# Performance work log

Hardware: AMD Instinct MI355X
Metric: run time of the kernel (lower is better)

## Reference

```python
import jax, jax.numpy as jnp
import numpy as np

B, S, HID = 2, 2048, 2048
H, KVH, D = 16, 4, 128
GROUPS = H // KVH  # 4


def apply_rotary(x, cos, sin):
    # x: [B, h, S, D]; cos/sin: [S, D//2]
    xr = x[..., 0::2]
    xi = x[..., 1::2]
    c = cos[None, None, :, :]
    s = sin[None, None, :, :]
    orr = xr * c - xi * s
    oi = xr * s + xi * c
    return jnp.stack([orr, oi], axis=-1).reshape(x.shape)


def setup_inputs() -> dict:
    key = jax.random.key(0)
    k0, k1, k2, k3, k4 = jax.random.split(key, 5)
    x = jax.random.normal(k0, (B, S, HID), dtype=jnp.float32)
    # real RoPE frequencies (llama-style), stored as [S, D//2, 2] = (cos, sin)
    inv_freq = 1.0 / (10000.0 ** (np.arange(0, D, 2, dtype=np.float32) / D))
    t = np.arange(S, dtype=np.float32)
    ang = np.outer(t, inv_freq)  # [S, D//2]
    freqs_cis = jnp.asarray(np.stack([np.cos(ang), np.sin(ang)], axis=-1), dtype=jnp.float32)
    sc = 0.02
    wq = jax.random.normal(k1, (HID, H * D), dtype=jnp.float32) * sc
    wk = jax.random.normal(k2, (HID, KVH * D), dtype=jnp.float32) * sc
    wv = jax.random.normal(k3, (HID, KVH * D), dtype=jnp.float32) * sc
    wo = jax.random.normal(k4, (H * D, HID), dtype=jnp.float32) * sc
    return {"x": x, "freqs_cis": freqs_cis, "wq": wq, "wk": wk, "wv": wv, "wo": wo}


def reference(x, freqs_cis, wq, wk, wv, wo):
    b, s, _ = x.shape
    cos, sin = freqs_cis[..., 0], freqs_cis[..., 1]
    q = (x @ wq).reshape(b, s, H, D).transpose(0, 2, 1, 3)    # [B,H,S,D]
    k = (x @ wk).reshape(b, s, KVH, D).transpose(0, 2, 1, 3)  # [B,KVH,S,D]
    v = (x @ wv).reshape(b, s, KVH, D).transpose(0, 2, 1, 3)
    q = apply_rotary(q, cos, sin)
    k = apply_rotary(k, cos, sin)
    # GQA expand: repeat kv heads into query-head groups
    k = jnp.repeat(k, GROUPS, axis=1)  # [B,H,S,D]
    v = jnp.repeat(v, GROUPS, axis=1)
    scale = 1.0 / jnp.sqrt(jnp.asarray(D, dtype=x.dtype))
    scores = jnp.einsum("bhqd,bhkd->bhqk", q, k) * scale
    causal = jnp.tril(jnp.ones((s, s), dtype=bool))
    scores = jnp.where(causal[None, None], scores, jnp.asarray(-jnp.inf, dtype=scores.dtype))
    attn = jax.nn.softmax(scores, axis=-1)
    out = jnp.einsum("bhqk,bhkd->bhqd", attn, v)
    out = out.transpose(0, 2, 1, 3).reshape(b, s, H * D)
    return out @ wo
```

## Files before the change

kernel.cpp:

```cpp
#include <hip/hip_runtime.h>
#include <hip/hip_bf16.h>

#define B_   2
#define S_   2048
#define HID_ 2048
#define H_   16
#define KVH_ 4
#define D_   128
#define M_   4096
#define NQKV 3072

typedef __attribute__((ext_vector_type(8))) short bf16x8;
typedef __attribute__((ext_vector_type(4))) float f32x4;
typedef const __attribute__((address_space(1))) unsigned int* gas_p;
typedef __attribute__((address_space(3))) unsigned int* las_p;

__device__ __forceinline__ unsigned short f2b(float f) {
    __hip_bfloat16 h = __float2bfloat16(f);
    return *reinterpret_cast<unsigned short*>(&h);
}
__device__ __forceinline__ float b2f(unsigned short u) {
    __hip_bfloat16 h;
    *reinterpret_cast<unsigned short*>(&h) = u;
    return __bfloat162float(h);
}

__global__ __launch_bounds__(256)
void convert_x(const float* __restrict__ x, unsigned short* __restrict__ xb) {
    int i = (blockIdx.x * 256 + threadIdx.x) * 4;
    float4 v = *(const float4*)(x + i);
    ushort4 o;
    o.x = f2b(v.x); o.y = f2b(v.y); o.z = f2b(v.z); o.w = f2b(v.w);
    *(ushort4*)(xb + i) = o;
}

__global__ __launch_bounds__(256)
void convert_w_t(const float* __restrict__ w, int N,
                 unsigned short* __restrict__ wt, int nbase) {
    __shared__ float tile[32][33];
    int tx = threadIdx.x & 31, ty = threadIdx.x >> 5;
    int n0 = blockIdx.x * 32, k0 = blockIdx.y * 32;
    #pragma unroll
    for (int j = 0; j < 4; j++)
        tile[ty + j*8][tx] = w[(size_t)(k0 + ty + j*8) * N + n0 + tx];
    __syncthreads();
    #pragma unroll
    for (int j = 0; j < 4; j++)
        wt[(size_t)(nbase + n0 + ty + j*8) * 2048 + k0 + tx] = f2b(tile[tx][ty + j*8]);
}

template<bool BF16OUT>
__global__ __launch_bounds__(256)
void gemm_bt(const unsigned short* __restrict__ A,
             const unsigned short* __restrict__ BT,
             void* __restrict__ Cv, int N) {
    __shared__ unsigned short As[128][32];
    __shared__ unsigned short Bs[128][32];

    int tid  = threadIdx.x;
    int lane = tid & 63, w = tid >> 6;
    int quad = lane >> 4, l15 = lane & 15;
    int row0 = blockIdx.y * 128, col0 = blockIdx.x * 128;
    int wm = (w & 1) * 64, wn = (w >> 1) * 64;

    f32x4 acc[4][4];
    const f32x4 zf = {0.f, 0.f, 0.f, 0.f};
    #pragma unroll
    for (int i = 0; i < 4; i++)
        #pragma unroll
        for (int j = 0; j < 4; j++) acc[i][j] = zf;

    const unsigned short* Arow = A  + (size_t)row0 * 2048;
    const unsigned short* Brow = BT + (size_t)col0 * 2048;

    for (int k0 = 0; k0 < 2048; k0 += 32) {
        #pragma unroll
        for (int it = 0; it < 2; it++) {
            int c = w * 128 + it * 64 + lane;
            int r = c >> 2, q8 = (c & 3) * 8;
            __builtin_amdgcn_global_load_lds(
                (gas_p)(Arow + (size_t)r * 2048 + k0 + q8),
                (las_p)((char*)&As[0][0] + (size_t)(w * 128 + it * 64) * 16),
                16, 0, 0);
            __builtin_amdgcn_global_load_lds(
                (gas_p)(Brow + (size_t)r * 2048 + k0 + q8),
                (las_p)((char*)&Bs[0][0] + (size_t)(w * 128 + it * 64) * 16),
                16, 0, 0);
        }
        __syncthreads();
        bf16x8 af[4], bf[4];
        #pragma unroll
        for (int i = 0; i < 4; i++) af[i] = *(const bf16x8*)&As[wm + i*16 + l15][quad * 8];
        #pragma unroll
        for (int j = 0; j < 4; j++) bf[j] = *(const bf16x8*)&Bs[wn + j*16 + l15][quad * 8];
        #pragma unroll
        for (int i = 0; i < 4; i++)
            #pragma unroll
            for (int j = 0; j < 4; j++)
                acc[i][j] = __builtin_amdgcn_mfma_f32_16x16x32_bf16(af[i], bf[j], acc[i][j], 0, 0, 0);
        __syncthreads();
    }

    #pragma unroll
    for (int i = 0; i < 4; i++)
        #pragma unroll
        for (int j = 0; j < 4; j++)
            #pragma unroll
            for (int r = 0; r < 4; r++) {
                size_t idx = (size_t)(row0 + wm + i*16 + quad*4 + r) * N + col0 + wn + j*16 + l15;
                if (BF16OUT) ((unsigned short*)Cv)[idx] = f2b(acc[i][j][r]);
                else         ((float*)Cv)[idx] = acc[i][j][r];
            }
}

__global__ __launch_bounds__(256)
void rope_kernel(unsigned short* __restrict__ qkv, const float* __restrict__ freqs) {
    int p = blockIdx.x * 256 + threadIdx.x;
    int m = p / 1280;
    int cp = p - m * 1280;
    int col = cp * 2;
    int s = m & (S_ - 1);
    int d = col & (D_ - 1);
    unsigned short* ptr = qkv + (size_t)m * NQKV + col;
    ushort2 uv = *(ushort2*)ptr;
    float xr = b2f(uv.x), xi = b2f(uv.y);
    float cs = freqs[s * 128 + d], sn = freqs[s * 128 + d + 1];
    ushort2 ov;
    ov.x = f2b(xr * cs - xi * sn);
    ov.y = f2b(xr * sn + xi * cs);
    *(ushort2*)ptr = ov;
}

__global__ __launch_bounds__(256)
void v_transpose(const unsigned short* __restrict__ qkv, unsigned short* __restrict__ vT) {
    __shared__ unsigned short tile[32][34];
    int tx = threadIdx.x & 31, ty = threadIdx.x >> 5;
    int s0 = blockIdx.x * 32;
    int c0 = blockIdx.y * 32;
    int b  = blockIdx.z;
    #pragma unroll
    for (int j = 0; j < 4; j++)
        tile[ty + j*8][tx] = qkv[(size_t)(b*2048 + s0 + ty + j*8) * NQKV + 2560 + c0 + tx];
    __syncthreads();
    #pragma unroll
    for (int j = 0; j < 4; j++)
        vT[(size_t)(b*512 + c0 + ty + j*8) * 2048 + s0 + tx] = tile[tx][ty + j*8];
}

__global__ __launch_bounds__(128)
void attn_mfma(const unsigned short* __restrict__ qkv,
               const unsigned short* __restrict__ vT,
               unsigned short* __restrict__ ao,
               unsigned short* __restrict__ wsP,
               float2* __restrict__ wsML) {
    __shared__ unsigned short Ks[64 * 128];
    __shared__ unsigned short Vt[128 * 64];

    int tid  = threadIdx.x;
    int lane = tid & 63, w = tid >> 6;
    int quad = lane >> 4, l15 = lane & 15;
    int bx = blockIdx.x, h = blockIdx.y, b = blockIdx.z;
    int hk = h >> 2;

    int qt, c;
    bool split = (bx < 32);
    if (split) { qt = 31 - (bx >> 1); c = bx & 1; }
    else       { qt = 47 - bx;        c = 0;      }
    int nt = qt + 1;
    int kt_begin = 0, kt_end = nt;
    if (split) {
        int nt0 = (nt + 1) >> 1;
        kt_begin = c ? nt0 : 0;
        kt_end   = c ? nt  : nt0;
    }
    int q0 = qt * 64;
    const float scale = 0.08838834764831845f;

    bf16x8 aq[2][4];
    #pragma unroll
    for (int qf = 0; qf < 2; qf++) {
        const unsigned short* qrow =
            qkv + (size_t)(b*2048 + q0 + w*32 + qf*16 + l15) * NQKV + h*128;
        #pragma unroll
        for (int k4 = 0; k4 < 4; k4++)
            aq[qf][k4] = *(const bf16x8*)(qrow + k4*32 + quad*8);
    }

    int koff[4][4];
    #pragma unroll
    for (int j = 0; j < 4; j++) {
        int row = ((j >> 1) * 32) + ((l15 >> 2) * 8) + ((j & 1) * 4) + (l15 & 3);
        #pragma unroll
        for (int k4 = 0; k4 < 4; k4++) {
            int slot = (k4 * 4 + quad) ^ (row & 15);
            koff[j][k4] = (row * 16 + slot) * 8;
        }
    }
    int vbase0 = (l15 * 8 + (quad ^ (l15 & 7))) * 8;
    int vbase1 = (l15 * 8 + ((4 + quad) ^ (l15 & 7))) * 8;

    const unsigned short* kb0 = qkv + (size_t)(b*2048) * NQKV + 2048 + hk*128;
    const unsigned short* vb0 = vT + (size_t)(b*512 + hk*128) * 2048;

    auto stage_k = [&](int kt) {
        #pragma unroll
        for (int it = 0; it < 8; it++) {
            int s = w * 512 + it * 64 + lane;
            int r = s >> 4, qp = s & 15;
            int q = qp ^ (r & 15);
            __builtin_amdgcn_global_load_lds(
                (gas_p)(kb0 + (size_t)(kt*64 + r) * NQKV + q * 8),
                (las_p)((char*)&Ks[0] + (w * 512 + it * 64) * 16),
                16, 0, 0);
        }
    };
    auto stage_v = [&](int kt) {
        #pragma unroll
        for (int it = 0; it < 8; it++) {
            int s = w * 512 + it * 64 + lane;
            int r = s >> 3, qp = s & 7;
            int q = qp ^ (r & 7);
            __builtin_amdgcn_global_load_lds(
                (gas_p)(vb0 + (size_t)r * 2048 + kt*64 + q * 8),
                (las_p)((char*)&Vt[0] + (w * 512 + it * 64) * 16),
                16, 0, 0);
        }
    };

    f32x4 o_acc[2][8];
    const f32x4 zf = {0.f, 0.f, 0.f, 0.f};
    #pragma unroll
    for (int qf = 0; qf < 2; qf++)
        #pragma unroll
        for (int jn = 0; jn < 8; jn++) o_acc[qf][jn] = zf;
    float m_i[2] = {-1e30f, -1e30f}, l_i[2] = {0.f, 0.f};
    int qglob[2] = {q0 + w*32 + l15, q0 + w*32 + 16 + l15};

    stage_k(kt_begin);
    for (int kt = kt_begin; kt < kt_end; kt++) {
        __syncthreads();
        stage_v(kt);

        f32x4 s_acc[2][4];
        #pragma unroll
        for (int j = 0; j < 4; j++) {
            s_acc[0][j] = zf; s_acc[1][j] = zf;
            #pragma unroll
            for (int k4 = 0; k4 < 4; k4++) {
                bf16x8 ak = *(const bf16x8*)&Ks[koff[j][k4]];
                s_acc[0][j] = __builtin_amdgcn_mfma_f32_16x16x32_bf16(ak, aq[0][k4], s_acc[0][j], 0, 0, 0);
                s_acc[1][j] = __builtin_amdgcn_mfma_f32_16x16x32_bf16(ak, aq[1][k4], s_acc[1][j], 0, 0, 0);
            }
        }

        bf16x8 pp[2][2];
        #pragma unroll
        for (int qf = 0; qf < 2; qf++) {
            float sv[4][4];
            #pragma unroll
            for (int j = 0; j < 4; j++)
                #pragma unroll
                for (int r = 0; r < 4; r++)
                    sv[j][r] = s_acc[qf][j][r] * scale;
            if (kt == qt) {
                #pragma unroll
                for (int j = 0; j < 4; j++)
                    #pragma unroll
                    for (int r = 0; r < 4; r++) {
                        int sloc = ((j >> 1) * 32) + quad*8 + ((j & 1) * 4) + r;
                        if (kt*64 + sloc > qglob[qf]) sv[j][r] = -1e30f;
                    }
            }
            float mx = sv[0][0];
            #pragma unroll
            for (int j = 0; j < 4; j++)
                #pragma unroll
                for (int r = 0; r < 4; r++) mx = fmaxf(mx, sv[j][r]);
            mx = fmaxf(mx, __shfl_xor(mx, 16));
            mx = fmaxf(mx, __shfl_xor(mx, 32));
            float mnew = fmaxf(m_i[qf], mx);
            float alpha = __expf(m_i[qf] - mnew);
            float rs = 0.f;
            float p[4][4];
            #pragma unroll
            for (int j = 0; j < 4; j++)
                #pragma unroll
                for (int r = 0; r < 4; r++) {
                    p[j][r] = __expf(sv[j][r] - mnew);
                    rs += p[j][r];
                }
            l_i[qf] = l_i[qf] * alpha + rs;
            m_i[qf] = mnew;
            #pragma unroll
            for (int jn = 0; jn < 8; jn++)
                #pragma unroll
                for (int r = 0; r < 4; r++) o_acc[qf][jn][r] *= alpha;
            #pragma unroll
            for (int r = 0; r < 4; r++) {
                pp[qf][0][r]     = (short)f2b(p[0][r]);
                pp[qf][0][r + 4] = (short)f2b(p[1][r]);
                pp[qf][1][r]     = (short)f2b(p[2][r]);
                pp[qf][1][r + 4] = (short)f2b(p[3][r]);
            }
        }

        __syncthreads();
        if (kt + 1 < kt_end) stage_k(kt + 1);

        #pragma unroll
        for (int jn = 0; jn < 8; jn++) {
            bf16x8 av0 = *(const bf16x8*)&Vt[jn*1024 + vbase0];
            bf16x8 av1 = *(const bf16x8*)&Vt[jn*1024 + vbase1];
            o_acc[0][jn] = __builtin_amdgcn_mfma_f32_16x16x32_bf16(av0, pp[0][0], o_acc[0][jn], 0, 0, 0);
            o_acc[0][jn] = __builtin_amdgcn_mfma_f32_16x16x32_bf16(av1, pp[0][1], o_acc[0][jn], 0, 0, 0);
            o_acc[1][jn] = __builtin_amdgcn_mfma_f32_16x16x32_bf16(av0, pp[1][0], o_acc[1][jn], 0, 0, 0);
            o_acc[1][jn] = __builtin_amdgcn_mfma_f32_16x16x32_bf16(av1, pp[1][1], o_acc[1][jn], 0, 0, 0);
        }
    }

    int pidx = ((qt - 16) * 16 + h) * 2 + b;
    #pragma unroll
    for (int qf = 0; qf < 2; qf++) {
        float lt = l_i[qf];
        lt += __shfl_xor(lt, 16);
        lt += __shfl_xor(lt, 32);
        float inv = 1.f / lt;
        int q_local = w*32 + qf*16 + l15;
        unsigned short* dst;
        if (!split || c == 1)
            dst = ao + (size_t)(b*2048 + q0 + q_local) * 2048 + h*128;
        else
            dst = wsP + (size_t)pidx * 8192 + q_local * 128;
        #pragma unroll
        for (int jn = 0; jn < 8; jn++) {
            ushort4 ov;
            ov.x = f2b(o_acc[qf][jn][0] * inv);
            ov.y = f2b(o_acc[qf][jn][1] * inv);
            ov.z = f2b(o_acc[qf][jn][2] * inv);
            ov.w = f2b(o_acc[qf][jn][3] * inv);
            *(ushort4*)(dst + jn*16 + quad*4) = ov;
        }
        if (split && quad == 0)
            wsML[(pidx*2 + c) * 64 + q_local] = make_float2(m_i[qf], lt);
    }
}

__global__ __launch_bounds__(256)
void merge_kernel(unsigned short* __restrict__ ao,
                  const unsigned short* __restrict__ wsP,
                  const float2* __restrict__ wsML) {
    int t = blockIdx.x * 256 + threadIdx.x;
    int d  = (t & 15) * 8;
    int h  = (t >> 4) & 15;
    int qg = 1024 + ((t >> 8) & 1023);
    int b  = t >> 18;
    int qt = qg >> 6, q_local = qg & 63;
    int pidx = ((qt - 16) * 16 + h) * 2 + b;

    float2 ml0 = wsML[(pidx*2 + 0) * 64 + q_local];
    float2 ml1 = wsML[(pidx*2 + 1) * 64 + q_local];
    float mm = fmaxf(ml0.x, ml1.x);
    float f0 = __expf(ml0.x - mm) * ml0.y;
    float f1 = __expf(ml1.x - mm) * ml1.y;
    float inv = 1.f / (f0 + f1);
    f0 *= inv; f1 *= inv;

    unsigned short* arow = ao + (size_t)(b*2048 + qg) * 2048 + h*128 + d;
    const unsigned short* prow = wsP + (size_t)pidx * 8192 + q_local * 128 + d;
    ushort4 a0 = *(ushort4*)arow,        a1 = *(ushort4*)(arow + 4);
    ushort4 p0 = *(const ushort4*)prow,  p1 = *(const ushort4*)(prow + 4);
    ushort4 o0, o1;
    o0.x = f2b(f1*b2f(a0.x) + f0*b2f(p0.x));
    o0.y = f2b(f1*b2f(a0.y) + f0*b2f(p0.y));
    o0.z = f2b(f1*b2f(a0.z) + f0*b2f(p0.z));
    o0.w = f2b(f1*b2f(a0.w) + f0*b2f(p0.w));
    o1.x = f2b(f1*b2f(a1.x) + f0*b2f(p1.x));
    o1.y = f2b(f1*b2f(a1.y) + f0*b2f(p1.y));
    o1.z = f2b(f1*b2f(a1.z) + f0*b2f(p1.z));
    o1.w = f2b(f1*b2f(a1.w) + f0*b2f(p1.w));
    *(ushort4*)arow = o0;
    *(ushort4*)(arow + 4) = o1;
}

extern "C" void kernel_launch(void* const* d_in, const int* in_sizes, int n_in,
                              void* d_out, int out_size, void* d_ws, size_t ws_size,
                              hipStream_t stream) {
    const float* x     = (const float*)d_in[0];
    const float* freqs = (const float*)d_in[1];
    const float* wq    = (const float*)d_in[2];
    const float* wk    = (const float*)d_in[3];
    const float* wv    = (const float*)d_in[4];
    const float* wo    = (const float*)d_in[5];
    float* out = (float*)d_out;

    char* ws = (char*)d_ws;
    unsigned short* xbf    = (unsigned short*)(ws);
    unsigned short* aobuf  = (unsigned short*)(ws);
    unsigned short* wqkvT  = (unsigned short*)(ws + (16u<<20));
    unsigned short* woT    = (unsigned short*)(ws + (28u<<20));
    unsigned short* qkvbuf = (unsigned short*)(ws + (36u<<20));
    unsigned short* vTbuf  = (unsigned short*)(ws + (60u<<20));
    unsigned short* wsP    = (unsigned short*)(ws + (16u<<20));
    float2*         wsML   = (float2*)(ws + (24u<<20));

    dim3 blk(256);
    convert_x<<<8192, blk, 0, stream>>>(x, xbf);
    convert_w_t<<<dim3(64, 64), blk, 0, stream>>>(wq, 2048, wqkvT, 0);
    convert_w_t<<<dim3(16, 64), blk, 0, stream>>>(wk,  512, wqkvT, 2048);
    convert_w_t<<<dim3(16, 64), blk, 0, stream>>>(wv,  512, wqkvT, 2560);
    convert_w_t<<<dim3(64, 64), blk, 0, stream>>>(wo, 2048, woT, 0);

    gemm_bt<true><<<dim3(NQKV/128, M_/128), blk, 0, stream>>>(xbf, wqkvT, qkvbuf, NQKV);
    rope_kernel<<<20480, blk, 0, stream>>>(qkvbuf, freqs);
    v_transpose<<<dim3(64, 16, 2), blk, 0, stream>>>(qkvbuf, vTbuf);
    attn_mfma<<<dim3(48, 16, 2), dim3(128), 0, stream>>>(qkvbuf, vTbuf, aobuf, wsP, wsML);
    merge_kernel<<<2048, blk, 0, stream>>>(aobuf, wsP, wsML);
    gemm_bt<false><<<dim3(2048/128, M_/128), blk, 0, stream>>>(aobuf, woT, out, 2048);
}
```

Before: 353.8 us.

## Fuse RoPE and V-transpose into QKV GEMM, share KV tiles across GQA heads

The four weight-conversion launches become one batched launch. RoPE and the V transpose move into the QKV GEMM epilogue, which removes two kernels and their round trips through global memory. The attention kernel now runs 512 threads per block covering all four query heads of a KV head, so each K/V tile staged in LDS is shared across the group. The split-KV scheme is reworked to use up to three chunks of 14 key tiles, and the merge kernel is generalised to match. The trade-offs are more uncoalesced scalar stores and freq loads in the GEMM epilogue and fewer, larger attention blocks.

After: 345.1 us. -2.5%, faster.

```diff
diff --git a/kernel.cpp b/kernel.cpp
--- a/kernel.cpp
+++ b/kernel.cpp
@@ -35,25 +35,35 @@
 }
 
 __global__ __launch_bounds__(256)
-void convert_w_t(const float* __restrict__ w, int N,
-                 unsigned short* __restrict__ wt, int nbase) {
+void convert_w_all(const float* __restrict__ wq, const float* __restrict__ wk,
+                   const float* __restrict__ wv, const float* __restrict__ wo,
+                   unsigned short* __restrict__ wqkvT,
+                   unsigned short* __restrict__ woT) {
     __shared__ float tile[32][33];
+    int z = blockIdx.z;
+    const float* w; int N, nbase; unsigned short* dst;
+    if (z == 0)      { w = wq; N = 2048; nbase = 0;    dst = wqkvT; }
+    else if (z == 1) { w = wk; N = 512;  nbase = 2048; dst = wqkvT; }
+    else if (z == 2) { w = wv; N = 512;  nbase = 2560; dst = wqkvT; }
+    else             { w = wo; N = 2048; nbase = 0;    dst = woT; }
+    int n0 = blockIdx.x * 32, k0 = blockIdx.y * 32;
+    if (n0 >= N) return;
     int tx = threadIdx.x & 31, ty = threadIdx.x >> 5;
-    int n0 = blockIdx.x * 32, k0 = blockIdx.y * 32;
     #pragma unroll
     for (int j = 0; j < 4; j++)
         tile[ty + j*8][tx] = w[(size_t)(k0 + ty + j*8) * N + n0 + tx];
     __syncthreads();
     #pragma unroll
     for (int j = 0; j < 4; j++)
-        wt[(size_t)(nbase + n0 + ty + j*8) * 2048 + k0 + tx] = f2b(tile[tx][ty + j*8]);
-}
-
-template<bool BF16OUT>
+        dst[(size_t)(nbase + n0 + ty + j*8) * 2048 + k0 + tx] = f2b(tile[tx][ty + j*8]);
+}
+
 __global__ __launch_bounds__(256)
-void gemm_bt(const unsigned short* __restrict__ A,
-             const unsigned short* __restrict__ BT,
-             void* __restrict__ Cv, int N) {
+void gemm_qkv(const unsigned short* __restrict__ A,
+              const unsigned short* __restrict__ BT,
+              unsigned short* __restrict__ qkv,
+              unsigned short* __restrict__ vT,
+              const float* __restrict__ freqs) {
     __shared__ unsigned short As[128][32];
     __shared__ unsigned short Bs[128][32];
 
@@ -101,53 +111,106 @@
         __syncthreads();
     }
 
+    bool isV = (col0 >= 2560);
+    #pragma unroll
+    for (int i = 0; i < 4; i++) {
+        int m0 = row0 + wm + i*16 + quad*4;
+        int s0 = m0 & 2047;
+        if (!isV) {
+            #pragma unroll
+            for (int j = 0; j < 4; j++) {
+                int col = col0 + wn + j*16 + l15;
+                int dd = (col & 127) & ~1;
+                bool odd = col & 1;
+                #pragma unroll
+                for (int r = 0; r < 4; r++) {
+                    int s = s0 + r;
+                    float cs = freqs[s*128 + dd];
+                    float sn = freqs[s*128 + dd + 1];
+                    float v  = acc[i][j][r];
+                    float pv = __shfl_xor(v, 1);
+                    float o  = odd ? (pv*sn + v*cs) : (v*cs - pv*sn);
+                    qkv[(size_t)(m0 + r) * NQKV + col] = f2b(o);
+                }
+            }
+        } else {
+            #pragma unroll
+            for (int j = 0; j < 4; j++) {
+                int col = col0 + wn + j*16 + l15;
+                int vrow = (m0 >> 11) * 512 + (col - 2560);
+                ushort4 ov;
+                ov.x = f2b(acc[i][j][0]);
+                ov.y = f2b(acc[i][j][1]);
+                ov.z = f2b(acc[i][j][2]);
+                ov.w = f2b(acc[i][j][3]);
+                *(ushort4*)(vT + (size_t)vrow * 2048 + s0) = ov;
+            }
+        }
+    }
+}
+
+__global__ __launch_bounds__(256)
+void gemm_out(const unsigned short* __restrict__ A,
+              const unsigned short* __restrict__ BT,
+              float* __restrict__ C, int N) {
+    __shared__ unsigned short As[128][32];
+    __shared__ unsigned short Bs[128][32];
+
+    int tid  = threadIdx.x;
+    int lane = tid & 63, w = tid >> 6;
+    int quad = lane >> 4, l15 = lane & 15;
+    int row0 = blockIdx.y * 128, col0 = blockIdx.x * 128;
+    int wm = (w & 1) * 64, wn = (w >> 1) * 64;
+
+    f32x4 acc[4][4];
+    const f32x4 zf = {0.f, 0.f, 0.f, 0.f};
     #pragma unroll
     for (int i = 0; i < 4; i++)
         #pragma unroll
+        for (int j = 0; j < 4; j++) acc[i][j] = zf;
+
+    const unsigned short* Arow = A  + (size_t)row0 * 2048;
+    const unsigned short* Brow = BT + (size_t)col0 * 2048;
+
+    for (int k0 = 0; k0 < 2048; k0 += 32) {
+        #pragma unroll
+        for (int it = 0; it < 2; it++) {
+            int c = w * 128 + it * 64 + lane;
+            int r = c >> 2, q8 = (c & 3) * 8;
+            __builtin_amdgcn_global_load_lds(
+                (gas_p)(Arow + (size_t)r * 2048 + k0 + q8),
+                (las_p)((char*)&As[0][0] + (size_t)(w * 128 + it * 64) * 16),
+                16, 0, 0);
+            __builtin_amdgcn_global_load_lds(
+                (gas_p)(Brow + (size_t)r * 2048 + k0 + q8),
+                (las_p)((char*)&Bs[0][0] + (size_t)(w * 128 + it * 64) * 16),
+                16, 0, 0);
+        }
+        __syncthreads();
+        bf16x8 af[4], bf[4];
+        #pragma unroll
+        for (int i = 0; i < 4; i++) af[i] = *(const bf16x8*)&As[wm + i*16 + l15][quad * 8];
+        #pragma unroll
+        for (int j = 0; j < 4; j++) bf[j] = *(const bf16x8*)&Bs[wn + j*16 + l15][quad * 8];
+        #pragma unroll
+        for (int i = 0; i < 4; i++)
+            #pragma unroll
+            for (int j = 0; j < 4; j++)
+                acc[i][j] = __builtin_amdgcn_mfma_f32_16x16x32_bf16(af[i], bf[j], acc[i][j], 0, 0, 0);
+        __syncthreads();
+    }
+
+    #pragma unroll
+    for (int i = 0; i < 4; i++)
+        #pragma unroll
         for (int j = 0; j < 4; j++)
             #pragma unroll
-            for (int r = 0; r < 4; r++) {
-                size_t idx = (size_t)(row0 + wm + i*16 + quad*4 + r) * N + col0 + wn + j*16 + l15;
-                if (BF16OUT) ((unsigned short*)Cv)[idx] = f2b(acc[i][j][r]);
-                else         ((float*)Cv)[idx] = acc[i][j][r];
-            }
-}
-
-__global__ __launch_bounds__(256)
-void rope_kernel(unsigned short* __restrict__ qkv, const float* __restrict__ freqs) {
-    int p = blockIdx.x * 256 + threadIdx.x;
-    int m = p / 1280;
-    int cp = p - m * 1280;
-    int col = cp * 2;
-    int s = m & (S_ - 1);
-    int d = col & (D_ - 1);
-    unsigned short* ptr = qkv + (size_t)m * NQKV + col;
-    ushort2 uv = *(ushort2*)ptr;
-    float xr = b2f(uv.x), xi = b2f(uv.y);
-    float cs = freqs[s * 128 + d], sn = freqs[s * 128 + d + 1];
-    ushort2 ov;
-    ov.x = f2b(xr * cs - xi * sn);
-    ov.y = f2b(xr * sn + xi * cs);
-    *(ushort2*)ptr = ov;
-}
-
-__global__ __launch_bounds__(256)
-void v_transpose(const unsigned short* __restrict__ qkv, unsigned short* __restrict__ vT) {
-    __shared__ unsigned short tile[32][34];
-    int tx = threadIdx.x & 31, ty = threadIdx.x >> 5;
-    int s0 = blockIdx.x * 32;
-    int c0 = blockIdx.y * 32;
-    int b  = blockIdx.z;
-    #pragma unroll
-    for (int j = 0; j < 4; j++)
-        tile[ty + j*8][tx] = qkv[(size_t)(b*2048 + s0 + ty + j*8) * NQKV + 2560 + c0 + tx];
-    __syncthreads();
-    #pragma unroll
-    for (int j = 0; j < 4; j++)
-        vT[(size_t)(b*512 + c0 + ty + j*8) * 2048 + s0 + tx] = tile[tx][ty + j*8];
-}
-
-__global__ __launch_bounds__(128)
+            for (int r = 0; r < 4; r++)
+                C[(size_t)(row0 + wm + i*16 + quad*4 + r) * N + col0 + wn + j*16 + l15]
+                    = acc[i][j][r];
+}
+
+__global__ __launch_bounds__(512)
 void attn_mfma(const unsigned short* __restrict__ qkv,
                const unsigned short* __restrict__ vT,
                unsigned short* __restrict__ ao,
@@ -159,20 +222,19 @@
     int tid  = threadIdx.x;
     int lane = tid & 63, w = tid >> 6;
     int quad = lane >> 4, l15 = lane & 15;
-    int bx = blockIdx.x, h = blockIdx.y, b = blockIdx.z;
-    int hk = h >> 2;
+    int hw = w >> 1, qhalf = w & 1;
+    int bx = blockIdx.x, hk = blockIdx.y, b = blockIdx.z;
+    int h = hk * 4 + hw;
 
     int qt, c;
-    bool split = (bx < 32);
-    if (split) { qt = 31 - (bx >> 1); c = bx & 1; }
-    else       { qt = 47 - bx;        c = 0;      }
+    if (bx < 12)      { qt = 31 - bx / 3;        c = bx % 3; }
+    else if (bx < 40) { qt = 27 - (bx - 12) / 2; c = (bx - 12) & 1; }
+    else              { qt = 53 - bx;            c = 0; }
     int nt = qt + 1;
-    int kt_begin = 0, kt_end = nt;
-    if (split) {
-        int nt0 = (nt + 1) >> 1;
-        kt_begin = c ? nt0 : 0;
-        kt_end   = c ? nt  : nt0;
-    }
+    int nch = (qt >= 28) ? 3 : (qt >= 14 ? 2 : 1);
+    int kt_begin = c * 14;
+    int kt_end = (nt < (c + 1) * 14) ? nt : (c + 1) * 14;
+    bool lastc = (c == nch - 1);
     int q0 = qt * 64;
     const float scale = 0.08838834764831845f;
 
@@ -180,7 +242,7 @@
     #pragma unroll
     for (int qf = 0; qf < 2; qf++) {
         const unsigned short* qrow =
-            qkv + (size_t)(b*2048 + q0 + w*32 + qf*16 + l15) * NQKV + h*128;
+            qkv + (size_t)(b*2048 + q0 + qhalf*32 + qf*16 + l15) * NQKV + h*128;
         #pragma unroll
         for (int k4 = 0; k4 < 4; k4++)
             aq[qf][k4] = *(const bf16x8*)(qrow + k4*32 + quad*8);
@@ -204,25 +266,25 @@
 
     auto stage_k = [&](int kt) {
         #pragma unroll
-        for (int it = 0; it < 8; it++) {
-            int s = w * 512 + it * 64 + lane;
+        for (int it = 0; it < 2; it++) {
+            int s = w * 128 + it * 64 + lane;
             int r = s >> 4, qp = s & 15;
             int q = qp ^ (r & 15);
             __builtin_amdgcn_global_load_lds(
                 (gas_p)(kb0 + (size_t)(kt*64 + r) * NQKV + q * 8),
-                (las_p)((char*)&Ks[0] + (w * 512 + it * 64) * 16),
+                (las_p)((char*)&Ks[0] + (w * 128 + it * 64) * 16),
                 16, 0, 0);
         }
     };
     auto stage_v = [&](int kt) {
         #pragma unroll
-        for (int it = 0; it < 8; it++) {
-            int s = w * 512 + it * 64 + lane;
+        for (int it = 0; it < 2; it++) {
+            int s = w * 128 + it * 64 + lane;
             int r = s >> 3, qp = s & 7;
             int q = qp ^ (r & 7);
             __builtin_amdgcn_global_load_lds(
                 (gas_p)(vb0 + (size_t)r * 2048 + kt*64 + q * 8),
-                (las_p)((char*)&Vt[0] + (w * 512 + it * 64) * 16),
+                (las_p)((char*)&Vt[0] + (w * 128 + it * 64) * 16),
                 16, 0, 0);
         }
     };
@@ -234,7 +296,7 @@
         #pragma unroll
         for (int jn = 0; jn < 8; jn++) o_acc[qf][jn] = zf;
     float m_i[2] = {-1e30f, -1e30f}, l_i[2] = {0.f, 0.f};
-    int qglob[2] = {q0 + w*32 + l15, q0 + w*32 + 16 + l15};
+    int qglob[2] = {q0 + qhalf*32 + l15, q0 + qhalf*32 + 16 + l15};
 
     stage_k(kt_begin);
     for (int kt = kt_begin; kt < kt_end; kt++) {
@@ -318,19 +380,23 @@
         }
     }
 
-    int pidx = ((qt - 16) * 16 + h) * 2 + b;
+    int pi = 0, mi = 0;
+    if (qt >= 14) {
+        if (qt < 28) { mi = (qt - 14) * 2 + c;       pi = qt - 14; }
+        else         { mi = 28 + (qt - 28) * 3 + c;  pi = 14 + (qt - 28) * 2 + c; }
+    }
     #pragma unroll
     for (int qf = 0; qf < 2; qf++) {
         float lt = l_i[qf];
         lt += __shfl_xor(lt, 16);
         lt += __shfl_xor(lt, 32);
         float inv = 1.f / lt;
-        int q_local = w*32 + qf*16 + l15;
+        int q_local = qhalf * 32 + qf * 16 + l15;
         unsigned short* dst;
-        if (!split || c == 1)
+        if (lastc)
             dst = ao + (size_t)(b*2048 + q0 + q_local) * 2048 + h*128;
         else
-            dst = wsP + (size_t)pidx * 8192 + q_local * 128;
+            dst = wsP + (size_t)(((pi * 8 + hk * 2 + b) * 4 + hw) * 64 + q_local) * 128;
         #pragma unroll
         for (int jn = 0; jn < 8; jn++) {
             ushort4 ov;
@@ -340,8 +406,9 @@
             ov.w = f2b(o_acc[qf][jn][3] * inv);
             *(ushort4*)(dst + jn*16 + quad*4) = ov;
         }
-        if (split && quad == 0)
-            wsML[(pidx*2 + c) * 64 + q_local] = make_float2(m_i[qf], lt);
+        if (qt >= 14 && quad == 0)
+            wsML[(mi * 8 + hk * 2 + b) * 256 + hw * 64 + q_local]
+                = make_float2(m_i[qf], lt);
     }
 }
 
@@ -350,34 +417,54 @@
                   const unsigned short* __restrict__ wsP,
                   const float2* __restrict__ wsML) {
     int t = blockIdx.x * 256 + threadIdx.x;
-    int d  = (t & 15) * 8;
-    int h  = (t >> 4) & 15;
-    int qg = 1024 + ((t >> 8) & 1023);
-    int b  = t >> 18;
-    int qt = qg >> 6, q_local = qg & 63;
-    int pidx = ((qt - 16) * 16 + h) * 2 + b;
-
-    float2 ml0 = wsML[(pidx*2 + 0) * 64 + q_local];
-    float2 ml1 = wsML[(pidx*2 + 1) * 64 + q_local];
-    float mm = fmaxf(ml0.x, ml1.x);
-    float f0 = __expf(ml0.x - mm) * ml0.y;
-    float f1 = __expf(ml1.x - mm) * ml1.y;
-    float inv = 1.f / (f0 + f1);
-    f0 *= inv; f1 *= inv;
-
-    unsigned short* arow = ao + (size_t)(b*2048 + qg) * 2048 + h*128 + d;
-    const unsigned short* prow = wsP + (size_t)pidx * 8192 + q_local * 128 + d;
-    ushort4 a0 = *(ushort4*)arow,        a1 = *(ushort4*)(arow + 4);
-    ushort4 p0 = *(const ushort4*)prow,  p1 = *(const ushort4*)(prow + 4);
+    int d = (t & 15) * 8;
+    int h = (t >> 4) & 15;
+    int rest = t >> 8;
+    int q_off = rest % 1152;
+    int b = rest / 1152;
+    int q = 896 + q_off;
+    int qt = q >> 6, q_local = q & 63;
+    int hk = h >> 2, hw = h & 3;
+    int nch = (qt >= 28) ? 3 : 2;
+
+    float mv[3], lv[3];
+    for (int cc = 0; cc < nch; cc++) {
+        int mi = (qt < 28) ? (qt - 14) * 2 + cc : 28 + (qt - 28) * 3 + cc;
+        float2 ml = wsML[(mi * 8 + hk * 2 + b) * 256 + hw * 64 + q_local];
+        mv[cc] = ml.x; lv[cc] = ml.y;
+    }
+    float M = mv[0];
+    for (int cc = 1; cc < nch; cc++) M = fmaxf(M, mv[cc]);
+    float f[3], S = 0.f;
+    for (int cc = 0; cc < nch; cc++) { f[cc] = __expf(mv[cc] - M) * lv[cc]; S += f[cc]; }
+    float inv = 1.f / S;
+
+    unsigned short* arow = ao + (size_t)(b*2048 + q) * 2048 + h*128 + d;
+    float outv[8];
+    {
+        ushort4 a0 = *(ushort4*)arow, a1 = *(ushort4*)(arow + 4);
+        float fl = f[nch-1];
+        outv[0] = fl*b2f(a0.x); outv[1] = fl*b2f(a0.y);
+        outv[2] = fl*b2f(a0.z); outv[3] = fl*b2f(a0.w);
+        outv[4] = fl*b2f(a1.x); outv[5] = fl*b2f(a1.y);
+        outv[6] = fl*b2f(a1.z); outv[7] = fl*b2f(a1.w);
+    }
+    for (int cc = 0; cc < nch - 1; cc++) {
+        int pi = (qt < 28) ? (qt - 14) : 14 + (qt - 28) * 2 + cc;
+        const unsigned short* prow =
+            wsP + (size_t)(((pi * 8 + hk * 2 + b) * 4 + hw) * 64 + q_local) * 128 + d;
+        ushort4 p0 = *(const ushort4*)prow, p1 = *(const ushort4*)(prow + 4);
+        float fc = f[cc];
+        outv[0] += fc*b2f(p0.x); outv[1] += fc*b2f(p0.y);
+        outv[2] += fc*b2f(p0.z); outv[3] += fc*b2f(p0.w);
+        outv[4] += fc*b2f(p1.x); outv[5] += fc*b2f(p1.y);
+        outv[6] += fc*b2f(p1.z); outv[7] += fc*b2f(p1.w);
+    }
     ushort4 o0, o1;
-    o0.x = f2b(f1*b2f(a0.x) + f0*b2f(p0.x));
-    o0.y = f2b(f1*b2f(a0.y) + f0*b2f(p0.y));
-    o0.z = f2b(f1*b2f(a0.z) + f0*b2f(p0.z));
-    o0.w = f2b(f1*b2f(a0.w) + f0*b2f(p0.w));
-    o1.x = f2b(f1*b2f(a1.x) + f0*b2f(p1.x));
-    o1.y = f2b(f1*b2f(a1.y) + f0*b2f(p1.y));
-    o1.z = f2b(f1*b2f(a1.z) + f0*b2f(p1.z));
-    o1.w = f2b(f1*b2f(a1.w) + f0*b2f(p1.w));
+    o0.x = f2b(outv[0]*inv); o0.y = f2b(outv[1]*inv);
+    o0.z = f2b(outv[2]*inv); o0.w = f2b(outv[3]*inv);
+    o1.x = f2b(outv[4]*inv); o1.y = f2b(outv[5]*inv);
+    o1.z = f2b(outv[6]*inv); o1.w = f2b(outv[7]*inv);
     *(ushort4*)arow = o0;
     *(ushort4*)(arow + 4) = o1;
 }
@@ -400,20 +487,14 @@
     unsigned short* woT    = (unsigned short*)(ws + (28u<<20));
     unsigned short* qkvbuf = (unsigned short*)(ws + (36u<<20));
     unsigned short* vTbuf  = (unsigned short*)(ws + (60u<<20));
-    unsigned short* wsP    = (unsigned short*)(ws + (16u<<20));
-    float2*         wsML   = (float2*)(ws + (24u<<20));
+    unsigned short* wsP  = (unsigned short*)(ws + (16u<<20));
+    float2*         wsML = (float2*)(ws + (16u<<20) + 176u*65536u);
 
     dim3 blk(256);
     convert_x<<<8192, blk, 0, stream>>>(x, xbf);
-    convert_w_t<<<dim3(64, 64), blk, 0, stream>>>(wq, 2048, wqkvT, 0);
-    convert_w_t<<<dim3(16, 64), blk, 0, stream>>>(wk,  512, wqkvT, 2048);
-    convert_w_t<<<dim3(16, 64), blk, 0, stream>>>(wv,  512, wqkvT, 2560);
-    convert_w_t<<<dim3(64, 64), blk, 0, stream>>>(wo, 2048, woT, 0);
-
-    gemm_bt<true><<<dim3(NQKV/128, M_/128), blk, 0, stream>>>(xbf, wqkvT, qkvbuf, NQKV);
-    rope_kernel<<<20480, blk, 0, stream>>>(qkvbuf, freqs);
-    v_transpose<<<dim3(64, 16, 2), blk, 0, stream>>>(qkvbuf, vTbuf);
-    attn_mfma<<<dim3(48, 16, 2), dim3(128), 0, stream>>>(qkvbuf, vTbuf, aobuf, wsP, wsML);
-    merge_kernel<<<2048, blk, 0, stream>>>(aobuf, wsP, wsML);
-    gemm_bt<false><<<dim3(2048/128, M_/128), blk, 0, stream>>>(aobuf, woT, out, 2048);
-}
+    convert_w_all<<<dim3(64, 64, 4), blk, 0, stream>>>(wq, wk, wv, wo, wqkvT, woT);
+    gemm_qkv<<<dim3(NQKV/128, M_/128), blk, 0, stream>>>(xbf, wqkvT, qkvbuf, vTbuf, freqs);
+    attn_mfma<<<dim3(54, 4, 2), dim3(512), 0, stream>>>(qkvbuf, vTbuf, aobuf, wsP, wsML);
+    merge_kernel<<<2304, blk, 0, stream>>>(aobuf, wsP, wsML);
+    gemm_out<<<dim3(2048/128, M_/128), blk, 0, stream>>>(aobuf, woT, out, 2048);
+}
```
